# Kernel optimization log

Measured on AMD Instinct MI355X. Metric: run time of the kernel, lower is better.

## Reference

```python
import jax, jax.numpy as jnp
from jax import lax
import numpy as np

DN = ('NCHW', 'OIHW', 'NCHW')

def conv(x, w, b, stride, pad):
    y = lax.conv_general_dilated(x, w, (stride, stride), [(pad, pad), (pad, pad)], dimension_numbers=DN)
    return y if b is None else y + b[None, :, None, None]

def conv_transpose(x, w, b):
    # torch ConvTranspose2d(k=4, s=2, p=1); w in torch layout (Cin, Cout, 4, 4)
    w_f = jnp.flip(w, (2, 3)).transpose(1, 0, 2, 3)  # -> OIHW, flipped
    y = lax.conv_general_dilated(x, w_f, (1, 1), [(2, 2), (2, 2)], lhs_dilation=(2, 2), dimension_numbers=DN)
    return y + b[None, :, None, None]

def res_stack(x, w3, w1, n_layers=2):
    # shared weights across layers (ModuleList([layer]*n) aliases one module)
    for _ in range(n_layers):
        h = conv(jax.nn.relu(x), w3, None, 1, 1)
        h = conv(jax.nn.relu(h), w1, None, 1, 0)
        x = x + h
    return jax.nn.relu(x)

def setup_inputs() -> dict:
    key = jax.random.key(0)
    ks = jax.random.split(key, 16)
    s = 0.02
    d = {
        'x': jax.random.normal(ks[0], (32, 3, 256, 256), jnp.float32),
        'enc_w1': jax.random.normal(ks[1], (128, 3, 4, 4), jnp.float32) * s,
        'enc_b1': jnp.zeros((128,), jnp.float32),
        'enc_w2': jax.random.normal(ks[2], (256, 128, 4, 4), jnp.float32) * s,
        'enc_b2': jnp.zeros((256,), jnp.float32),
        'enc_w3': jax.random.normal(ks[3], (512, 256, 4, 4), jnp.float32) * s,
        'enc_b3': jnp.zeros((512,), jnp.float32),
        'enc_res_w3': jax.random.normal(ks[4], (32, 512, 3, 3), jnp.float32) * s,
        'enc_res_w1': jax.random.normal(ks[5], (512, 32, 1, 1), jnp.float32) * s,
        'prevq_w': jax.random.normal(ks[6], (64, 512, 1, 1), jnp.float32) * s,
        'prevq_b': jnp.zeros((64,), jnp.float32),
        'emb': jax.random.normal(ks[7], (512, 64), jnp.float32),
        'dec_w1': jax.random.normal(ks[8], (64, 256, 4, 4), jnp.float32) * s,
        'dec_b1': jnp.zeros((256,), jnp.float32),
        'dec_res_w3': jax.random.normal(ks[9], (32, 256, 3, 3), jnp.float32) * s,
        'dec_res_w1': jax.random.normal(ks[10], (256, 32, 1, 1), jnp.float32) * s,
        'dec_w2': jax.random.normal(ks[11], (256, 128, 4, 4), jnp.float32) * s,
        'dec_b2': jnp.zeros((128,), jnp.float32),
        'dec_w3': jax.random.normal(ks[12], (128, 3, 4, 4), jnp.float32) * s,
        'dec_b3': jnp.zeros((3,), jnp.float32),
    }
    return d

def vqvae_fwd(x, enc_w1, enc_b1, enc_w2, enc_b2, enc_w3, enc_b3, enc_res_w3, enc_res_w1,
              prevq_w, prevq_b, emb, dec_w1, dec_b1, dec_res_w3, dec_res_w1,
              dec_w2, dec_b2, dec_w3, dec_b3):
    # encoder
    z = jax.nn.relu(conv(x, enc_w1, enc_b1, 2, 1))
    z = jax.nn.relu(conv(z, enc_w2, enc_b2, 2, 1))
    z = conv(z, enc_w3, enc_b3, 2, 1)
    z = res_stack(z, enc_res_w3, enc_res_w1)
    z_e = conv(z, prevq_w, prevq_b, 1, 0)  # (B, D=64, 32, 32)
    # vector quantiser
    B, C, H, W = z_e.shape
    x_flat = z_e.reshape(B, C, H * W).transpose(0, 2, 1)  # (B, HW, D)
    d2 = (jnp.sum(x_flat ** 2, -1, keepdims=True)
          - 2.0 * jnp.einsum('bnd,kd->bnk', x_flat, emb)
          + jnp.sum(emb ** 2, -1))
    idx = jnp.argmin(d2, axis=2)  # (B, HW)
    z_q_flat = emb[idx]  # (B, HW, D)
    z_q = z_q_flat.transpose(0, 2, 1).reshape(B, C, H, W)
    sg = lax.stop_gradient
    q_loss = jnp.mean((sg(z_q_flat) - x_flat) ** 2) + jnp.mean((z_q_flat - sg(x_flat)) ** 2)
    # decoder
    y = conv_transpose(z_q, dec_w1, dec_b1)  # (B, 256, 64, 64)
    y = res_stack(y, dec_res_w3, dec_res_w1)
    y = jax.nn.relu(conv_transpose(y, dec_w2, dec_b2))
    y = conv_transpose(y, dec_w3, dec_b3)  # (B, 3, 256, 256)
    return y, q_loss

def reference(x, enc_w1, enc_b1, enc_w2, enc_b2, enc_w3, enc_b3, enc_res_w3, enc_res_w1,
              prevq_w, prevq_b, emb, dec_w1, dec_b1, dec_res_w3, dec_res_w1,
              dec_w2, dec_b2, dec_w3, dec_b3):
    return vqvae_fwd(x, enc_w1, enc_b1, enc_w2, enc_b2, enc_w3, enc_b3, enc_res_w3, enc_res_w1,
                     prevq_w, prevq_b, emb, dec_w1, dec_b1, dec_res_w3, dec_res_w1,
                     dec_w2, dec_b2, dec_w3, dec_b3)
```

## Files before the change

kernel.cpp:

```cpp
#include <hip/hip_runtime.h>
#include <hip/hip_bf16.h>

typedef __attribute__((ext_vector_type(8))) short short8;
typedef __attribute__((ext_vector_type(4))) float f32x4;
typedef __attribute__((ext_vector_type(4))) unsigned int uint4v;

__device__ __forceinline__ unsigned short f2bf(float f) {
  unsigned u = __builtin_bit_cast(unsigned, f);
  u = (u + 0x7FFFu + ((u >> 16) & 1u)) >> 16;
  return (unsigned short)u;
}
__device__ __forceinline__ float bf2f(unsigned short h) {
  unsigned u = ((unsigned)h) << 16;
  return __builtin_bit_cast(float, u);
}
__device__ __forceinline__ unsigned pk_bf16(float a, float b) {
  __hip_bfloat162 h = __float22bfloat162_rn(make_float2(a, b));
  unsigned u;
  __builtin_memcpy(&u, &h, 4);
  return u;
}

template<int TMT, int MT, int MODE, bool SPLIT, bool RELU_IN, bool RELU_OUT, bool BIAS, bool ACCUM>
__global__ __launch_bounds__(256, 4) void k_mfconv(
    const float* __restrict__ in, const unsigned short* __restrict__ wp,
    const float* __restrict__ bias, float* __restrict__ out,
    int Ci, int inW, int inH, int pWSH, int pHWSH,
    int Co, int ntap, int ntt,
    unsigned syp, unsigned sxp,
    int outW, int outHW) {
  const int tid  = threadIdx.x;
  const int lane = tid & 63, wave = tid >> 6;
  const int pW  = 1 << pWSH;
  const int pHW = 1 << pHWSH;
  const int inHW = inW * inH;
  const int nk32 = Ci >> 5;
  const int KS   = (nk32 >= 2) ? 2 : 1;
  const int NITS = 4 * KS;
  const int cpt  = nk32 / KS;
  const int total = ntap * cpt;
  constexpr int TT = TMT * MT;

  int bx = blockIdx.x;
  const int gx = gridDim.x;
  if ((gx & 7) == 0) bx = (bx & 7) * (gx >> 3) + (bx >> 3);
  const int n0  = bx * 64;
  const int coG = blockIdx.y;
  const int ph  = (MODE == 1) ? blockIdx.z : 0;
  const int tap0 = (MODE == 1) ? ph * 4 : 0;
  const int pdy = ph >> 1, pdx = ph & 1;

  constexpr int NPL = SPLIT ? 2 : 1;
  constexpr int PL = 64 * 70;
  __shared__ __align__(16) unsigned short Bs[2 * NPL * PL];

  const int px  = lane;
  const int p   = n0 + px;
  const int img = p >> pHWSH;
  const int rem = p & (pHW - 1);
  const int y   = rem >> pWSH;
  const int x   = rem & (pW - 1);
  const size_t base_img = (size_t)img * Ci * inHW;

  constexpr int NTO = (TMT == 4) ? 4 : 2;
  const int mt0 = (TMT == 4) ? wave : (wave & 1);
  const int ntb = (TMT == 4) ? 0 : ((wave >> 1) * 2);
  f32x4 acc[MT * NTO];
#pragma unroll
  for (int u = 0; u < MT * NTO; ++u) acc[u] = (f32x4){0.f, 0.f, 0.f, 0.f};

  const int cp = wave;
  float v[16];

  auto ldr = [&](int tap_, int chunk_) {
    const int T = tap0 + tap_;
    const int dy = (int)((syp >> (2 * T)) & 3u) - 1;
    const int dx = (int)((sxp >> (2 * T)) & 3u) - 1;
    const int ys = (MODE == 2) ? (2 * y + dy) : (y + dy);
    const int xs = (MODE == 2) ? (2 * x + dx) : (x + dx);
    const bool ok = ((unsigned)ys < (unsigned)inH) && ((unsigned)xs < (unsigned)inW);
    const float* __restrict__ ipb = in + base_img + (ptrdiff_t)ys * inW + xs;
    const int ci0 = chunk_ * (KS * 32);
#pragma unroll
    for (int it2 = 0; it2 < 8; ++it2) {
      if (it2 >= NITS) break;
      const int cl = 2 * (cp + 4 * it2);
      float a = 0.f, b = 0.f;
      if (ok) {
        a = ipb[(size_t)(ci0 + cl) * inHW];
        b = ipb[(size_t)(ci0 + cl + 1) * inHW];
      }
      if (RELU_IN) { a = fmaxf(a, 0.f); b = fmaxf(b, 0.f); }
      v[2 * it2] = a; v[2 * it2 + 1] = b;
    }
  };
  auto pwr = [&](int b) {
#pragma unroll
    for (int it2 = 0; it2 < 8; ++it2) {
      if (it2 >= NITS) break;
      const int cl = 2 * (cp + 4 * it2);
      float a = v[2 * it2], c = v[2 * it2 + 1];
      unsigned hp = pk_bf16(a, c);
      *(unsigned*)&Bs[(b * NPL) * PL + px * 70 + cl] = hp;
      if (SPLIT) {
        float h0 = bf2f((unsigned short)hp), h1 = bf2f((unsigned short)(hp >> 16));
        *(unsigned*)&Bs[(b * NPL + 1) * PL + px * 70 + cl] = pk_bf16(a - h0, c - h1);
      }
    }
  };

  ldr(0, 0);
  pwr(0);
  __syncthreads();

  int tap = 0, chunk = 0;
  for (int it = 0; it < total; ++it) {
    const int b = it & 1;
    const int T = tap0 + tap;
    int tap2 = tap, chunk2 = chunk + 1;
    if (chunk2 == cpt) { chunk2 = 0; tap2 = tap + 1; }
    const bool more = (it + 1 < total);
    if (more) ldr(tap2, chunk2);
#pragma unroll
    for (int s = 0; s < 2; ++s) {
      if (s >= KS) break;
      const int cic = chunk * KS + s;
      short8 ah[MT], al[MT];
#pragma unroll
      for (int m = 0; m < MT; ++m) {
        const int mtm = mt0 + m * TMT;
        size_t abase;
        if (SPLIT) abase = ((((size_t)coG * ntt + T) * nk32 + cic) * 2 * TT + mtm) * 512;
        else       abase = ((((size_t)coG * ntt + T) * nk32 + cic) * TT + mtm) * 512;
        ah[m] = *(const short8*)(wp + abase + (size_t)lane * 8);
        if (SPLIT) al[m] = *(const short8*)(wp + abase + (size_t)TT * 512 + (size_t)lane * 8);
      }
      short8 bh[NTO], bl[NTO];
#pragma unroll
      for (int u = 0; u < NTO; ++u) {
        const int row = 16 * (ntb + u) + (lane & 15);
        const unsigned* bp = (const unsigned*)&Bs[(b * NPL) * PL + row * 70 + s * 32 + (lane >> 4) * 8];
        uint4v hv = {bp[0], bp[1], bp[2], bp[3]};
        bh[u] = __builtin_bit_cast(short8, hv);
        if (SPLIT) {
          const unsigned* bpl = bp + (PL >> 1);
          uint4v lv = {bpl[0], bpl[1], bpl[2], bpl[3]};
          bl[u] = __builtin_bit_cast(short8, lv);
        }
      }
#pragma unroll
      for (int m = 0; m < MT; ++m)
#pragma unroll
        for (int u = 0; u < NTO; ++u) {
          f32x4 a = acc[m * NTO + u];
          a = __builtin_amdgcn_mfma_f32_16x16x32_bf16(ah[m], bh[u], a, 0, 0, 0);
          if (SPLIT) {
            a = __builtin_amdgcn_mfma_f32_16x16x32_bf16(al[m], bh[u], a, 0, 0, 0);
            a = __builtin_amdgcn_mfma_f32_16x16x32_bf16(ah[m], bl[u], a, 0, 0, 0);
          }
          acc[m * NTO + u] = a;
        }
    }
    if (more) {
      pwr(b ^ 1);
      __syncthreads();
    }
    tap = tap2; chunk = chunk2;
  }

#pragma unroll
  for (int m = 0; m < MT; ++m) {
    const int mtm = mt0 + m * TMT;
#pragma unroll
    for (int u = 0; u < NTO; ++u) {
      const int nt = ntb + u;
      const int pn = n0 + nt * 16 + (lane & 15);
      const int img2 = pn >> pHWSH;
      const int rem2 = pn & (pHW - 1);
      const int y2 = rem2 >> pWSH, x2 = rem2 & (pW - 1);
      int oy, ox;
      if (MODE == 1) { oy = 2 * y2 + pdy; ox = 2 * x2 + pdx; }
      else           { oy = y2;           ox = x2; }
#pragma unroll
      for (int r = 0; r < 4; ++r) {
        const int co = coG * (TT * 16) + mtm * 16 + (lane >> 4) * 4 + r;
        float val = acc[m * NTO + u][r];
        if (BIAS) val += bias[co];
        if (RELU_OUT) val = fmaxf(val, 0.f);
        size_t oi = ((size_t)img2 * Co + co) * outHW + (size_t)oy * outW + ox;
        if (ACCUM) out[oi] += val; else out[oi] = val;
      }
    }
  }
}

__global__ __launch_bounds__(256, 4) void k_mfenc1(
    const float* __restrict__ in, const unsigned short* __restrict__ wp,
    const float* __restrict__ bias, float* __restrict__ out) {
  const int tid = threadIdx.x, lane = tid & 63, wave = tid >> 6;
  int bx = blockIdx.x;
  const int gx = gridDim.x;
  if ((gx & 7) == 0) bx = (bx & 7) * (gx >> 3) + (bx >> 3);
  const int n0 = bx * 64;
  const int p = n0 + lane;
  const int img = p >> 14;
  const int rem = p & 16383;
  const int y = rem >> 7, x = rem & 127;
  __shared__ __align__(16) unsigned short Bs[2 * 4480];
  const float* __restrict__ ib = in + (size_t)img * 3 * 65536;
#pragma unroll
  for (int i = 0; i < 8; ++i) {
    const int kk0 = 2 * (wave + 4 * i);
    float vv[2];
#pragma unroll
    for (int q = 0; q < 2; ++q) {
      const int kk = kk0 + q;
      const int tap = kk >> 2, c = kk & 3;
      const int iy = 2 * y + (tap >> 2) - 1, ix = 2 * x + (tap & 3) - 1;
      const bool ok = (c < 3) && ((unsigned)iy < 256u) && ((unsigned)ix < 256u);
      vv[q] = ok ? ib[((size_t)c << 16) + (size_t)iy * 256 + ix] : 0.f;
    }
    unsigned hp = pk_bf16(vv[0], vv[1]);
    *(unsigned*)&Bs[lane * 70 + kk0] = hp;
    float h0 = bf2f((unsigned short)hp), h1 = bf2f((unsigned short)(hp >> 16));
    *(unsigned*)&Bs[4480 + lane * 70 + kk0] = pk_bf16(vv[0] - h0, vv[1] - h1);
  }
  __syncthreads();

  f32x4 acc[8];
#pragma unroll
  for (int u = 0; u < 8; ++u) acc[u] = (f32x4){0.f, 0.f, 0.f, 0.f};
#pragma unroll
  for (int s = 0; s < 2; ++s) {
    short8 ah[2], al[2];
#pragma unroll
    for (int m = 0; m < 2; ++m) {
      const int mtm = wave + m * 4;
      size_t abase = (((size_t)s * 2 + 0) * 8 + mtm) * 512;
      ah[m] = *(const short8*)(wp + abase + (size_t)lane * 8);
      al[m] = *(const short8*)(wp + abase + 8 * 512 + (size_t)lane * 8);
    }
    short8 bh[4], bl[4];
#pragma unroll
    for (int u = 0; u < 4; ++u) {
      const int row = 16 * u + (lane & 15);
      const unsigned* bp = (const unsigned*)&Bs[row * 70 + s * 32 + (lane >> 4) * 8];
      uint4v hv = {bp[0], bp[1], bp[2], bp[3]};
      bh[u] = __builtin_bit_cast(short8, hv);
      const unsigned* bpl = bp + 2240;
      uint4v lv = {bpl[0], bpl[1], bpl[2], bpl[3]};
      bl[u] = __builtin_bit_cast(short8, lv);
    }
#pragma unroll
    for (int m = 0; m < 2; ++m)
#pragma unroll
      for (int u = 0; u < 4; ++u) {
        f32x4 a = acc[m * 4 + u];
        a = __builtin_amdgcn_mfma_f32_16x16x32_bf16(ah[m], bh[u], a, 0, 0, 0);
        a = __builtin_amdgcn_mfma_f32_16x16x32_bf16(al[m], bh[u], a, 0, 0, 0);
        a = __builtin_amdgcn_mfma_f32_16x16x32_bf16(ah[m], bl[u], a, 0, 0, 0);
        acc[m * 4 + u] = a;
      }
  }
#pragma unroll
  for (int m = 0; m < 2; ++m)
#pragma unroll
    for (int u = 0; u < 4; ++u) {
      const int pn = n0 + u * 16 + (lane & 15);
      const int img2 = pn >> 14;
      const int rem2 = pn & 16383;
#pragma unroll
      for (int r = 0; r < 4; ++r) {
        const int co = (wave + m * 4) * 16 + (lane >> 4) * 4 + r;
        float val = fmaxf(acc[m * 4 + u][r] + bias[co], 0.f);
        out[((size_t)img2 * 128 + co) * 16384 + rem2] = val;
      }
    }
}

template<bool SPLIT>
__global__ __launch_bounds__(256) void k_pack_o(
    const float* __restrict__ w, unsigned short* __restrict__ p,
    int Co, int Ci, int ntap, int TMT, int E) {
  int i = blockIdx.x * 256 + threadIdx.x;
  if (i >= E) return;
  const int NC = Ci >> 5;
  int j = i & 7, lane = (i >> 3) & 63, r = i >> 9;
  int mt = r % TMT; r /= TMT;
  int sp = 0;
  if (SPLIT) { sp = r % 2; r /= 2; }
  int cic = r % NC; r /= NC;
  int T = r % ntap; int coG = r / ntap;
  int co = coG * (TMT * 16) + mt * 16 + (lane & 15);
  int ci = cic * 32 + (lane >> 4) * 8 + j;
  float wv = w[((size_t)co * Ci + ci) * ntap + T];
  unsigned short hv = f2bf(wv);
  p[i] = (SPLIT && sp == 1) ? f2bf(wv - bf2f(hv)) : hv;
}

__global__ __launch_bounds__(256) void k_pack_ct(
    const float* __restrict__ w, unsigned short* __restrict__ p,
    int Ci, int Co, int TMT, int E) {
  int i = blockIdx.x * 256 + threadIdx.x;
  if (i >= E) return;
  const int NC = Ci >> 5;
  int j = i & 7, lane = (i >> 3) & 63, r = i >> 9;
  int mt = r % TMT; r /= TMT;
  int cic = r % NC; r /= NC;
  int T = r % 16;   int coG = r / 16;
  int phx = T >> 2, t = T & 3;
  int dy = phx >> 1, dx = phx & 1, ty = t >> 1, tx = t & 1;
  int ky = 2 * ty + 1 - dy, kx = 2 * tx + 1 - dx;
  int co = coG * (TMT * 16) + mt * 16 + (lane & 15);
  int ci = cic * 32 + (lane >> 4) * 8 + j;
  p[i] = f2bf(w[(((size_t)ci * Co + co) * 4 + ky) * 4 + kx]);
}

__global__ __launch_bounds__(256) void k_pack_e1(
    const float* __restrict__ w, unsigned short* __restrict__ p) {
  int i = blockIdx.x * 256 + threadIdx.x;
  int j = i & 7, lane = (i >> 3) & 63, r = i >> 9;
  int mt = r % 8; r /= 8;
  int sp = r % 2; r /= 2;
  int cic = r;
  int co = mt * 16 + (lane & 15);
  int kk = cic * 32 + (lane >> 4) * 8 + j;
  int tap = kk >> 2, c = kk & 3;
  float wv = (c < 3) ? w[(((size_t)co * 3 + c) * 4 + (tap >> 2)) * 4 + (tap & 3)] : 0.f;
  unsigned short hv = f2bf(wv);
  p[i] = (sp == 1) ? f2bf(wv - bf2f(hv)) : hv;
}

template<int COB, bool RELU_OUT>
__global__ __launch_bounds__(256) void k_conv4(
    const float* __restrict__ in, const float* __restrict__ w,
    const float* __restrict__ bias, float* __restrict__ out,
    int N, int Ci, int Hi, int Wi, int Co) {
  const int Ho = Hi >> 1, Wo = Wi >> 1;
  const int ow = blockIdx.x * 16 + (threadIdx.x & 15);
  const int oh = blockIdx.y * 16 + (threadIdx.x >> 4);
  const int zcnt = Co / COB;
  const int co0 = (blockIdx.z % zcnt) * COB;
  const int n   = blockIdx.z / zcnt;
  if (oh >= Ho || ow >= Wo) return;
  const float* __restrict__ ip = in + (size_t)n * Ci * Hi * Wi;
  float acc[COB];
#pragma unroll
  for (int j = 0; j < COB; ++j) acc[j] = bias[co0 + j];
  const int ih0 = 2 * oh - 1, iw0 = 2 * ow - 1;
  for (int ci = 0; ci < Ci; ++ci) {
    const float* __restrict__ ic = ip + (size_t)ci * Hi * Wi;
    float v[16];
#pragma unroll
    for (int kh = 0; kh < 4; ++kh) {
      const int ih = ih0 + kh;
      const bool hok = (unsigned)ih < (unsigned)Hi;
      const float* __restrict__ irow = ic + (long)ih * Wi;
#pragma unroll
      for (int kw = 0; kw < 4; ++kw) {
        const int iw = iw0 + kw;
        v[kh * 4 + kw] = (hok && (unsigned)iw < (unsigned)Wi) ? irow[iw] : 0.f;
      }
    }
#pragma unroll
    for (int j = 0; j < COB; ++j) {
      const float* __restrict__ wc = w + ((size_t)(co0 + j) * Ci + ci) * 16;
#pragma unroll
      for (int t = 0; t < 16; ++t) acc[j] = fmaf(v[t], wc[t], acc[j]);
    }
  }
#pragma unroll
  for (int j = 0; j < COB; ++j) {
    float a = acc[j];
    if (RELU_OUT) a = fmaxf(a, 0.f);
    out[(((size_t)n * Co + co0 + j) * Ho + oh) * Wo + ow] = a;
  }
}

template<int COB, bool RELU_IN, int CSPLIT>
__global__ __launch_bounds__(256) void k_conv3(
    const float* __restrict__ in, const float* __restrict__ w,
    float* __restrict__ out, int N, int Ci, int H, int W, int Co) {
  const int ow = blockIdx.x * 16 + (threadIdx.x & 15);
  const int oh = blockIdx.y * 16 + (threadIdx.x >> 4);
  const int zcnt = Co / COB;
  const int z = blockIdx.z;
  const int cs  = z % CSPLIT;
  const int co0 = ((z / CSPLIT) % zcnt) * COB;
  const int n   = z / (CSPLIT * zcnt);
  if (oh >= H || ow >= W) return;
  const int CPS = Ci / CSPLIT;
  const float* __restrict__ ip = in + (size_t)n * Ci * H * W;
  float acc[COB];
#pragma unroll
  for (int j = 0; j < COB; ++j) acc[j] = 0.f;
  for (int ci = cs * CPS; ci < (cs + 1) * CPS; ++ci) {
    const float* __restrict__ ic = ip + (size_t)ci * H * W;
    float v[9];
#pragma unroll
    for (int kh = 0; kh < 3; ++kh) {
      const int ih = oh - 1 + kh;
      const bool hok = (unsigned)ih < (unsigned)H;
      const float* __restrict__ irow = ic + (long)ih * W;
#pragma unroll
      for (int kw = 0; kw < 3; ++kw) {
        const int iw = ow - 1 + kw;
        float t = (hok && (unsigned)iw < (unsigned)W) ? irow[iw] : 0.f;
        if (RELU_IN) t = fmaxf(t, 0.f);
        v[kh * 3 + kw] = t;
      }
    }
#pragma unroll
    for (int j = 0; j < COB; ++j) {
      const float* __restrict__ wc = w + ((size_t)(co0 + j) * Ci + ci) * 9;
#pragma unroll
      for (int t = 0; t < 9; ++t) acc[j] = fmaf(v[t], wc[t], acc[j]);
    }
  }
#pragma unroll
  for (int j = 0; j < COB; ++j) {
    size_t oi = (((size_t)n * Co + co0 + j) * H + oh) * W + ow;
    if (CSPLIT > 1) atomicAdd(&out[oi], acc[j]);
    else out[oi] = acc[j];
  }
}

template<int COB, bool RELU_IN, bool ACCUM>
__global__ __launch_bounds__(256) void k_conv1(
    const float* __restrict__ in, const float* __restrict__ w,
    const float* __restrict__ bias, float* __restrict__ out,
    int N, int Ci, int P, int Co) {
  const int p = blockIdx.x * 256 + threadIdx.x;
  const int co0 = blockIdx.y * COB;
  const int n = blockIdx.z;
  if (p >= P) return;
  float acc[COB];
#pragma unroll
  for (int j = 0; j < COB; ++j) acc[j] = bias ? bias[co0 + j] : 0.f;
  const float* __restrict__ ip = in + (size_t)n * Ci * P + p;
#pragma unroll 8
  for (int ci = 0; ci < Ci; ++ci) {
    float v = ip[(size_t)ci * P];
    if (RELU_IN) v = fmaxf(v, 0.f);
#pragma unroll
    for (int j = 0; j < COB; ++j)
      acc[j] = fmaf(v, w[(size_t)(co0 + j) * Ci + ci], acc[j]);
  }
#pragma unroll
  for (int j = 0; j < COB; ++j) {
    size_t oi = ((size_t)n * Co + co0 + j) * P + p;
    if (ACCUM) out[oi] += acc[j]; else out[oi] = acc[j];
  }
}

template<int COB, bool RELU_IN, bool RELU_OUT>
__global__ __launch_bounds__(256) void k_convT(
    const float* __restrict__ in, const float* __restrict__ w,
    const float* __restrict__ bias, float* __restrict__ out,
    int N, int Ci, int Hi, int Wi, int Co) {
  const int Ho = Hi * 2, Wo = Wi * 2;
  const int x = blockIdx.x * 16 + (threadIdx.x & 15);
  const int y = blockIdx.y * 16 + (threadIdx.x >> 4);
  const int zcnt = Co / COB;
  const int co0 = (blockIdx.z % zcnt) * COB;
  const int n   = blockIdx.z / zcnt;
  if (x >= Wi || y >= Hi) return;
  const float* __restrict__ ip = in + (size_t)n * Ci * Hi * Wi;
  float a00[COB], a01[COB], a10[COB], a11[COB];
#pragma unroll
  for (int j = 0; j < COB; ++j) {
    float b = bias[co0 + j];
    a00[j] = b; a01[j] = b; a10[j] = b; a11[j] = b;
  }
  const bool r0 = y > 0, r2 = y + 1 < Hi, c0 = x > 0, c2 = x + 1 < Wi;
#pragma unroll 2
  for (int ci = 0; ci < Ci; ++ci) {
    const float* __restrict__ ic = ip + (size_t)ci * Hi * Wi + (size_t)y * Wi + x;
    float v00 = 0.f, v01 = 0.f, v02 = 0.f, v10 = 0.f, v12 = 0.f,
          v20 = 0.f, v21 = 0.f, v22 = 0.f;
    float v11 = ic[0];
    if (c0) v10 = ic[-1];
    if (c2) v12 = ic[1];
    if (r0) { v01 = ic[-Wi]; if (c0) v00 = ic[-Wi - 1]; if (c2) v02 = ic[-Wi + 1]; }
    if (r2) { v21 = ic[Wi];  if (c0) v20 = ic[Wi - 1];  if (c2) v22 = ic[Wi + 1]; }
    if (RELU_IN) {
      v00 = fmaxf(v00, 0.f); v01 = fmaxf(v01, 0.f); v02 = fmaxf(v02, 0.f);
      v10 = fmaxf(v10, 0.f); v11 = fmaxf(v11, 0.f); v12 = fmaxf(v12, 0.f);
      v20 = fmaxf(v20, 0.f); v21 = fmaxf(v21, 0.f); v22 = fmaxf(v22, 0.f);
    }
#pragma unroll
    for (int j = 0; j < COB; ++j) {
      const float* __restrict__ wc = w + ((size_t)ci * Co + co0 + j) * 16;
      a00[j] = fmaf(v11, wc[5],  fmaf(v10, wc[7],  fmaf(v01, wc[13], fmaf(v00, wc[15], a00[j]))));
      a01[j] = fmaf(v12, wc[4],  fmaf(v11, wc[6],  fmaf(v02, wc[12], fmaf(v01, wc[14], a01[j]))));
      a10[j] = fmaf(v21, wc[1],  fmaf(v20, wc[3],  fmaf(v11, wc[9],  fmaf(v10, wc[11], a10[j]))));
      a11[j] = fmaf(v22, wc[0],  fmaf(v21, wc[2],  fmaf(v12, wc[8],  fmaf(v11, wc[10], a11[j]))));
    }
  }
#pragma unroll
  for (int j = 0; j < COB; ++j) {
    size_t b = ((size_t)n * Co + co0 + j) * Ho;
    float o00 = a00[j], o01 = a01[j], o10 = a10[j], o11 = a11[j];
    if (RELU_OUT) {
      o00 = fmaxf(o00, 0.f); o01 = fmaxf(o01, 0.f);
      o10 = fmaxf(o10, 0.f); o11 = fmaxf(o11, 0.f);
    }
    out[(b + 2 * y) * Wo + 2 * x]         = o00;
    out[(b + 2 * y) * Wo + 2 * x + 1]     = o01;
    out[(b + 2 * y + 1) * Wo + 2 * x]     = o10;
    out[(b + 2 * y + 1) * Wo + 2 * x + 1] = o11;
  }
}

__global__ __launch_bounds__(256, 2) void k_vq(
    const float* __restrict__ ze, const float* __restrict__ emb,
    float* __restrict__ zq, float* __restrict__ loss) {
  __shared__ float e2s[512];
  const int tid = threadIdx.x;
  for (int k = tid; k < 512; k += 256) {
    const f32x4* e4 = (const f32x4*)(emb + (size_t)k * 64);
    float s = 0.f;
#pragma unroll
    for (int dq = 0; dq < 16; ++dq) {
      f32x4 ev = e4[dq];
      s = fmaf(ev[0], ev[0], s); s = fmaf(ev[1], ev[1], s);
      s = fmaf(ev[2], ev[2], s); s = fmaf(ev[3], ev[3], s);
    }
    e2s[k] = s;
  }
  __syncthreads();
  const int p = blockIdx.x * 256 + tid;
  const int n = p >> 10, px = p & 1023;
  float xv[64];
  const float* __restrict__ zp = ze + (size_t)n * 64 * 1024 + px;
#pragma unroll
  for (int d = 0; d < 64; ++d) xv[d] = zp[(size_t)d * 1024];
  float best = 1e30f; int bi = 0;
  for (int k = 0; k < 512; ++k) {
    const f32x4* e4 = (const f32x4*)(emb + (size_t)k * 64);
    float dot = 0.f;
#pragma unroll
    for (int dq = 0; dq < 16; ++dq) {
      f32x4 ev = e4[dq];
      dot = fmaf(xv[4 * dq],     ev[0], dot);
      dot = fmaf(xv[4 * dq + 1], ev[1], dot);
      dot = fmaf(xv[4 * dq + 2], ev[2], dot);
      dot = fmaf(xv[4 * dq + 3], ev[3], dot);
    }
    float sc = fmaf(-2.f, dot, e2s[k]);
    if (sc < best) { best = sc; bi = k; }
  }
  const float* __restrict__ eb = emb + (size_t)bi * 64;
  float* __restrict__ qp = zq + (size_t)n * 64 * 1024 + px;
  float l = 0.f;
#pragma unroll
  for (int d = 0; d < 64; ++d) {
    float ev = eb[d];
    qp[(size_t)d * 1024] = ev;
    float df = ev - xv[d];
    l = fmaf(df, df, l);
  }
#pragma unroll
  for (int off = 32; off > 0; off >>= 1) l += __shfl_down(l, off, 64);
  if ((tid & 63) == 0) atomicAdd(loss, l * (2.f / 2097152.f));
}

__global__ __launch_bounds__(64) void k_vq64(
    const float* __restrict__ ze, const float* __restrict__ emb,
    float* __restrict__ zq, float* __restrict__ loss,
    int N, int P, int K) {
  const int t = blockIdx.x * 64 + threadIdx.x;
  if (t >= N * P) return;
  const int n = t / P, p = t % P;
  float xv[64];
  const float* __restrict__ zp = ze + (size_t)n * 64 * P + p;
#pragma unroll
  for (int d = 0; d < 64; ++d) xv[d] = zp[(size_t)d * P];
  float best = 1e30f; int bi = 0;
  for (int k = 0; k < K; ++k) {
    const float* __restrict__ e = emb + (size_t)k * 64;
    float dot = 0.f, e2 = 0.f;
#pragma unroll
    for (int d = 0; d < 64; ++d) {
      float ev = e[d];
      dot = fmaf(xv[d], ev, dot);
      e2  = fmaf(ev, ev, e2);
    }
    float score = e2 - 2.f * dot;
    if (score < best) { best = score; bi = k; }
  }
  const float* __restrict__ eb = emb + (size_t)bi * 64;
  float* __restrict__ qp = zq + (size_t)n * 64 * P + p;
  float l = 0.f;
#pragma unroll
  for (int d = 0; d < 64; ++d) {
    float ev = eb[d];
    qp[(size_t)d * P] = ev;
    float df = ev - xv[d];
    l = fmaf(df, df, l);
  }
#pragma unroll
  for (int off = 32; off > 0; off >>= 1) l += __shfl_down(l, off, 64);
  if ((threadIdx.x & 63) == 0) atomicAdd(loss, l * (2.f / 2097152.f));
}

extern "C" void kernel_launch(void* const* d_in, const int* in_sizes, int n_in,
                              void* d_out, int out_size, void* d_ws, size_t ws_size,
                              hipStream_t stream) {
  const float* x    = (const float*)d_in[0];
  const float* ew1  = (const float*)d_in[1];
  const float* eb1  = (const float*)d_in[2];
  const float* ew2  = (const float*)d_in[3];
  const float* eb2  = (const float*)d_in[4];
  const float* ew3  = (const float*)d_in[5];
  const float* eb3  = (const float*)d_in[6];
  const float* erw3 = (const float*)d_in[7];
  const float* erw1 = (const float*)d_in[8];
  const float* pqw  = (const float*)d_in[9];
  const float* pqb  = (const float*)d_in[10];
  const float* emb  = (const float*)d_in[11];
  const float* dw1  = (const float*)d_in[12];
  const float* db1  = (const float*)d_in[13];
  const float* drw3 = (const float*)d_in[14];
  const float* drw1 = (const float*)d_in[15];
  const float* dw2  = (const float*)d_in[16];
  const float* db2  = (const float*)d_in[17];
  const float* dw3  = (const float*)d_in[18];
  const float* db3  = (const float*)d_in[19];
  float* out = (float*)d_out;
  char*  ws  = (char*)d_ws;
  float* loss = out + 6291456;
  const size_t MiB = 1048576ull, KiB = 1024ull;

  dim3 blk(256);
  hipMemsetAsync(loss, 0, 4, stream);

  unsigned syct = 0, sxct = 0;
  for (int T = 0; T < 16; ++T) {
    int phx = T >> 2, dy = phx >> 1, dx = phx & 1, t = T & 3, ty = t >> 1, tx = t & 1;
    int sy = (dy == 0) ? (ty ? -1 : 0) : (ty ? 0 : 1);
    int sx = (dx == 0) ? (tx ? -1 : 0) : (tx ? 0 : 1);
    syct |= (unsigned)(sy + 1) << (2 * T);
    sxct |= (unsigned)(sx + 1) << (2 * T);
  }
  unsigned syc3 = 0, sxc3 = 0;
  for (int t = 0; t < 9; ++t) {
    syc3 |= (unsigned)(t / 3) << (2 * t);
    sxc3 |= (unsigned)(t % 3) << (2 * t);
  }
  unsigned syc4 = 0, sxc4 = 0;
  for (int t = 0; t < 16; ++t) {
    syc4 |= (unsigned)(t / 4) << (2 * t);
    sxc4 |= (unsigned)(t % 4) << (2 * t);
  }
  const unsigned sy1 = 1, sx1 = 1;

  auto packs = [&](char* PB) {
    unsigned short* e2p   = (unsigned short*)(PB);
    unsigned short* e3p   = (unsigned short*)(PB + 2048 * KiB);
    unsigned short* erc3p = (unsigned short*)(PB + 10240 * KiB);
    unsigned short* erc1p = (unsigned short*)(PB + 10816 * KiB);
    unsigned short* pqp   = (unsigned short*)(PB + 10880 * KiB);
    unsigned short* d1p   = (unsigned short*)(PB + 11008 * KiB);
    unsigned short* d2p   = (unsigned short*)(PB + 11520 * KiB);
    unsigned short* dc3p  = (unsigned short*)(PB + 12544 * KiB);
    unsigned short* dc1p  = (unsigned short*)(PB + 12688 * KiB);
    unsigned short* e1p   = (unsigned short*)(PB + 12704 * KiB);
    k_pack_o<true ><<<dim3(1048576 / 256), blk, 0, stream>>>(ew2,  e2p,  256, 128, 16, 8, 1048576);
    k_pack_o<true ><<<dim3(4194304 / 256), blk, 0, stream>>>(ew3,  e3p,  512, 256, 16, 8, 4194304);
    k_pack_o<true ><<<dim3(294912 / 256),  blk, 0, stream>>>(erw3, erc3p, 32, 512,  9, 2, 294912);
    k_pack_o<true ><<<dim3(32768 / 256),   blk, 0, stream>>>(erw1, erc1p, 512, 32,  1, 8, 32768);
    k_pack_o<true ><<<dim3(65536 / 256),   blk, 0, stream>>>(pqw,  pqp,   64, 512,  1, 4, 65536);
    k_pack_ct<<<dim3(262144 / 256), blk, 0, stream>>>(dw1, d1p, 64, 256, 8, 262144);
    k_pack_ct<<<dim3(524288 / 256), blk, 0, stream>>>(dw2, d2p, 256, 128, 8, 524288);
    k_pack_o<false><<<dim3(73728 / 256),   blk, 0, stream>>>(drw3, dc3p,  32, 256,  9, 2, 73728);
    k_pack_o<false><<<dim3(8192 / 256),    blk, 0, stream>>>(drw1, dc1p, 256, 32,  1, 8, 8192);
    k_pack_e1<<<dim3(256), blk, 0, stream>>>(ew1, e1p);
  };

  if (ws_size >= 498ull * MiB) {
    float* z1 = (float*)ws;
    float* z2 = (float*)(ws + 256 * MiB);
    float* z3 = (float*)(ws + 384 * MiB);
    float* h  = (float*)(ws + 448 * MiB);
    float* ze = (float*)(ws + 452 * MiB);
    float* zq = (float*)(ws + 460 * MiB);
    float* hd = (float*)(ws + 468 * MiB);
    char*  PB = ws + 484 * MiB;
    unsigned short* e2p   = (unsigned short*)(PB);
    unsigned short* e3p   = (unsigned short*)(PB + 2048 * KiB);
    unsigned short* erc3p = (unsigned short*)(PB + 10240 * KiB);
    unsigned short* erc1p = (unsigned short*)(PB + 10816 * KiB);
    unsigned short* pqp   = (unsigned short*)(PB + 10880 * KiB);
    unsigned short* d1p   = (unsigned short*)(PB + 11008 * KiB);
    unsigned short* d2p   = (unsigned short*)(PB + 11520 * KiB);
    unsigned short* dc3p  = (unsigned short*)(PB + 12544 * KiB);
    unsigned short* dc1p  = (unsigned short*)(PB + 12688 * KiB);
    unsigned short* e1p   = (unsigned short*)(PB + 12704 * KiB);
    packs(PB);

    k_mfenc1<<<dim3(8192), blk, 0, stream>>>(x, e1p, eb1, z1);
    k_mfconv<4, 2, 2, true, false, true, true, false><<<dim3(2048, 2), blk, 0, stream>>>(
        z1, e2p, eb2, z2, 128, 128, 128, 6, 12, 256, 16, 16, syc4, sxc4, 64, 4096);
    k_mfconv<4, 2, 2, true, false, false, true, false><<<dim3(512, 4), blk, 0, stream>>>(
        z2, e3p, eb3, z3, 256, 64, 64, 5, 10, 512, 16, 16, syc4, sxc4, 32, 1024);
    for (int i = 0; i < 2; ++i) {
      k_mfconv<2, 1, 0, true, true, false, false, false><<<dim3(512, 1), blk, 0, stream>>>(
          z3, erc3p, nullptr, h, 512, 32, 32, 5, 10, 32, 9, 9, syc3, sxc3, 32, 1024);
      k_mfconv<4, 2, 0, true, true, false, false, true><<<dim3(512, 4), blk, 0, stream>>>(
          h, erc1p, nullptr, z3, 32, 32, 32, 5, 10, 512, 1, 1, sy1, sx1, 32, 1024);
    }
    k_mfconv<4, 1, 0, true, true, false, true, false><<<dim3(512, 1), blk, 0, stream>>>(
        z3, pqp, pqb, ze, 512, 32, 32, 5, 10, 64, 1, 1, sy1, sx1, 32, 1024);
    k_vq<<<dim3(128), blk, 0, stream>>>(ze, emb, zq, loss);
    float* y1 = (float*)(ws + 256 * MiB);
    float* y2 = (float*)ws;
    k_mfconv<4, 2, 1, false, false, false, true, false><<<dim3(512, 2, 4), blk, 0, stream>>>(
        zq, d1p, db1, y1, 64, 32, 32, 5, 10, 256, 4, 16, syct, sxct, 64, 4096);
    for (int i = 0; i < 2; ++i) {
      k_mfconv<2, 1, 0, false, true, false, false, false><<<dim3(2048, 1), blk, 0, stream>>>(
          y1, dc3p, nullptr, hd, 256, 64, 64, 6, 12, 32, 9, 9, syc3, sxc3, 64, 4096);
      k_mfconv<4, 2, 0, false, true, false, false, true><<<dim3(2048, 2), blk, 0, stream>>>(
          hd, dc1p, nullptr, y1, 32, 64, 64, 6, 12, 256, 1, 1, sy1, sx1, 64, 4096);
    }
    k_mfconv<4, 2, 1, false, true, true, true, false><<<dim3(2048, 1, 4), blk, 0, stream>>>(
        y1, d2p, db2, y2, 256, 64, 64, 6, 12, 128, 4, 16, syct, sxct, 128, 16384);
    k_convT<3, false, false><<<dim3(8, 8, 32), blk, 0, stream>>>(y2, dw3, db3, out, 32, 128, 128, 128, 3);
    return;
  }

  if (ws_size >= 128ull * MiB) {
    float* z3  = (float*)ws;
    float* h   = (float*)(ws + 64 * MiB);
    float* ze  = (float*)(ws + 68 * MiB);
    float* zq  = (float*)(ws + 100 * MiB);
    char*  PB  = ws + 115 * MiB;
    unsigned short* e2p   = (unsigned short*)(PB);
    unsigned short* e3p   = (unsigned short*)(PB + 2048 * KiB);
    unsigned short* erc3p = (unsigned short*)(PB + 10240 * KiB);
    unsigned short* erc1p = (unsigned short*)(PB + 10816 * KiB);
    unsigned short* pqp   = (unsigned short*)(PB + 10880 * KiB);
    unsigned short* d1p   = (unsigned short*)(PB + 11008 * KiB);
    unsigned short* d2p   = (unsigned short*)(PB + 11520 * KiB);
    unsigned short* dc3p  = (unsigned short*)(PB + 12544 * KiB);
    unsigned short* dc1p  = (unsigned short*)(PB + 12688 * KiB);
    unsigned short* e1p   = (unsigned short*)(PB + 12704 * KiB);
    packs(PB);

    const int NE = 4;
    float* z1c = (float*)(ws + 64 * MiB);
    float* z2c = (float*)(ws + 96 * MiB);
    for (int n0 = 0; n0 < 32; n0 += NE) {
      const float* xb = x + (size_t)n0 * 3 * 65536;
      float* z3b = z3 + (size_t)n0 * 512 * 1024;
      k_mfenc1<<<dim3(NE * 256), blk, 0, stream>>>(xb, e1p, eb1, z1c);
      k_mfconv<4, 2, 2, true, false, true, true, false><<<dim3(256, 2), blk, 0, stream>>>(
          z1c, e2p, eb2, z2c, 128, 128, 128, 6, 12, 256, 16, 16, syc4, sxc4, 64, 4096);
      k_mfconv<4, 2, 2, true, false, false, true, false><<<dim3(64, 4), blk, 0, stream>>>(
          z2c, e3p, eb3, z3b, 256, 64, 64, 5, 10, 512, 16, 16, syc4, sxc4, 32, 1024);
    }
    for (int i = 0; i < 2; ++i) {
      k_mfconv<2, 1, 0, true, true, false, false, false><<<dim3(512, 1), blk, 0, stream>>>(
          z3, erc3p, nullptr, h, 512, 32, 32, 5, 10, 32, 9, 9, syc3, sxc3, 32, 1024);
      k_mfconv<4, 2, 0, true, true, false, false, true><<<dim3(512, 4), blk, 0, stream>>>(
          h, erc1p, nullptr, z3, 32, 32, 32, 5, 10, 512, 1, 1, sy1, sx1, 32, 1024);
    }
    k_mfconv<4, 1, 0, true, true, false, true, false><<<dim3(512, 1), blk, 0, stream>>>(
        z3, pqp, pqb, ze, 512, 32, 32, 5, 10, 64, 1, 1, sy1, sx1, 32, 1024);
    k_vq<<<dim3(128), blk, 0, stream>>>(ze, emb, zq, loss);

    const int ND = 8;
    float* y1c = (float*)ws;
    float* hd  = (float*)(ws + 32 * MiB);
    float* y2c = (float*)(ws + 36 * MiB);
    for (int c = 0; c < 32; c += ND) {
      const float* zqb = zq + (size_t)c * 64 * 1024;
      float* outb = out + (size_t)c * 3 * 65536;
      k_mfconv<4, 2, 1, false, false, false, true, false><<<dim3(128, 2, 4), blk, 0, stream>>>(
          zqb, d1p, db1, y1c, 64, 32, 32, 5, 10, 256, 4, 16, syct, sxct, 64, 4096);
      for (int i = 0; i < 2; ++i) {
        k_mfconv<2, 1, 0, false, true, false, false, false><<<dim3(512, 1), blk, 0, stream>>>(
            y1c, dc3p, nullptr, hd, 256, 64, 64, 6, 12, 32, 9, 9, syc3, sxc3, 64, 4096);
        k_mfconv<4, 2, 0, false, true, false, false, true><<<dim3(512, 2), blk, 0, stream>>>(
            hd, dc1p, nullptr, y1c, 32, 64, 64, 6, 12, 256, 1, 1, sy1, sx1, 64, 4096);
      }
      k_mfconv<4, 2, 1, false, true, true, true, false><<<dim3(512, 1, 4), blk, 0, stream>>>(
          y1c, d2p, db2, y2c, 256, 64, 64, 6, 12, 128, 4, 16, syct, sxct, 128, 16384);
      k_convT<3, false, false><<<dim3(8, 8, ND), blk, 0, stream>>>(y2c, dw3, db3, outb, ND, 128, 128, 128, 3);
    }
    return;
  }

  const size_t PER_IMG = 12582912ull;
  int NB = (int)(ws_size / PER_IMG);
  if (NB > 32) NB = 32;
  if (NB < 1)  NB = 1;

  for (int n0 = 0; n0 < 32; n0 += NB) {
    const int nb = (32 - n0 < NB) ? (32 - n0) : NB;
    const float* xb   = x   + (size_t)n0 * 3 * 65536;
    float*       outb = out + (size_t)n0 * 3 * 65536;

    float* z1 = (float*)ws;
    float* z2 = (float*)(ws + (size_t)NB * 8388608ull);
    float* z3 = (float*)ws;
    char*  tb = ws + (size_t)NB * 2097152ull;
    float* he = (float*)tb;
    float* ze = (float*)(tb + (size_t)NB * 131072ull);
    float* zq = (float*)(tb + (size_t)NB * 393216ull);
    float* hd = (float*)(tb + (size_t)NB * 655360ull);
    float* y1 = z2;
    float* y2 = (float*)ws;

    k_conv4<4, true ><<<dim3(8, 8, nb * 32), blk, 0, stream>>>(xb, ew1, eb1, z1, nb,   3, 256, 256, 128);
    k_conv4<4, true ><<<dim3(4, 4, nb * 64), blk, 0, stream>>>(z1, ew2, eb2, z2, nb, 128, 128, 128, 256);
    k_conv4<4, false><<<dim3(2, 2, nb * 128), blk, 0, stream>>>(z2, ew3, eb3, z3, nb, 256,  64,  64, 512);
    for (int i = 0; i < 2; ++i) {
      k_conv3<4, true, 1><<<dim3(2, 2, nb * 8), blk, 0, stream>>>(z3, erw3, he, nb, 512, 32, 32, 32);
      k_conv1<8, true, true><<<dim3(4, 64, nb), blk, 0, stream>>>(he, erw1, nullptr, z3, nb, 32, 1024, 512);
    }
    k_conv1<8, true, false><<<dim3(4, 8, nb), blk, 0, stream>>>(z3, pqw, pqb, ze, nb, 512, 1024, 64);
    k_vq64<<<dim3(nb * 16), dim3(64), 0, stream>>>(ze, emb, zq, loss, nb, 1024, 512);
    k_convT<4, false, false><<<dim3(2, 2, nb * 64), blk, 0, stream>>>(zq, dw1, db1, y1, nb,  64, 32, 32, 256);
    for (int i = 0; i < 2; ++i) {
      k_conv3<4, true, 1><<<dim3(4, 4, nb * 8), blk, 0, stream>>>(y1, drw3, hd, nb, 256, 64, 64, 32);
      k_conv1<8, true, true><<<dim3(16, 32, nb), blk, 0, stream>>>(hd, drw1, nullptr, y1, nb, 32, 4096, 256);
    }
    k_convT<4, true, true ><<<dim3(4, 4, nb * 32), blk, 0, stream>>>(y1, dw2, db2, y2, nb, 256, 64, 64, 128);
    k_convT<1, false, false><<<dim3(8, 8, nb * 3), blk, 0, stream>>>(y2, dw3, db3, outb, nb, 128, 128, 128, 3);
  }
}
```

Measured before the change: 4.290 ms.

## Split-K low-occupancy convs with atomics; run final ConvTranspose on MFMA path

```diff
diff --git a/kernel.cpp b/kernel.cpp
--- a/kernel.cpp
+++ b/kernel.cpp
@@ -21,14 +21,14 @@
   return u;
 }
 
-template<int TMT, int MT, int MODE, bool SPLIT, bool RELU_IN, bool RELU_OUT, bool BIAS, bool ACCUM>
+template<int TMT, int MT, int MODE, int ZSP, bool SPLIT, bool RELU_IN, bool RELU_OUT, bool BIAS, int SM>
 __global__ __launch_bounds__(256, 4) void k_mfconv(
     const float* __restrict__ in, const unsigned short* __restrict__ wp,
     const float* __restrict__ bias, float* __restrict__ out,
     int Ci, int inW, int inH, int pWSH, int pHWSH,
     int Co, int ntap, int ntt,
     unsigned syp, unsigned sxp,
-    int outW, int outHW) {
+    int outW, int outHW, int CoSt) {
   const int tid  = threadIdx.x;
   const int lane = tid & 63, wave = tid >> 6;
   const int pW  = 1 << pWSH;
@@ -50,6 +50,13 @@
   const int tap0 = (MODE == 1) ? ph * 4 : 0;
   const int pdy = ph >> 1, pdx = ph & 1;
 
+  int it0 = 0, itEnd = total;
+  if (MODE != 1 && ZSP > 1) {
+    const int per = total / ZSP;
+    it0 = blockIdx.z * per;
+    itEnd = it0 + per;
+  }
+
   constexpr int NPL = SPLIT ? 2 : 1;
   constexpr int PL = 64 * 70;
   __shared__ __align__(16) unsigned short Bs[2 * NPL * PL];
@@ -109,17 +116,17 @@
     }
   };
 
-  ldr(0, 0);
+  int tap = it0 / cpt, chunk = it0 % cpt;
+  ldr(tap, chunk);
   pwr(0);
   __syncthreads();
 
-  int tap = 0, chunk = 0;
-  for (int it = 0; it < total; ++it) {
-    const int b = it & 1;
+  for (int it = it0; it < itEnd; ++it) {
+    const int b = (it - it0) & 1;
     const int T = tap0 + tap;
     int tap2 = tap, chunk2 = chunk + 1;
     if (chunk2 == cpt) { chunk2 = 0; tap2 = tap + 1; }
-    const bool more = (it + 1 < total);
+    const bool more = (it + 1 < itEnd);
     if (more) ldr(tap2, chunk2);
 #pragma unroll
     for (int s = 0; s < 2; ++s) {
@@ -184,11 +191,15 @@
 #pragma unroll
       for (int r = 0; r < 4; ++r) {
         const int co = coG * (TT * 16) + mtm * 16 + (lane >> 4) * 4 + r;
-        float val = acc[m * NTO + u][r];
-        if (BIAS) val += bias[co];
-        if (RELU_OUT) val = fmaxf(val, 0.f);
-        size_t oi = ((size_t)img2 * Co + co) * outHW + (size_t)oy * outW + ox;
-        if (ACCUM) out[oi] += val; else out[oi] = val;
+        if (co < CoSt) {
+          float val = acc[m * NTO + u][r];
+          if (BIAS) val += bias[co];
+          if (RELU_OUT) val = fmaxf(val, 0.f);
+          size_t oi = ((size_t)img2 * Co + co) * outHW + (size_t)oy * outW + ox;
+          if (SM == 0) out[oi] = val;
+          else if (SM == 1) out[oi] += val;
+          else atomicAdd(&out[oi], val);
+        }
       }
     }
   }
@@ -300,7 +311,7 @@
 
 __global__ __launch_bounds__(256) void k_pack_ct(
     const float* __restrict__ w, unsigned short* __restrict__ p,
-    int Ci, int Co, int TMT, int E) {
+    int Ci, int CoR, int TMT, int E) {
   int i = blockIdx.x * 256 + threadIdx.x;
   if (i >= E) return;
   const int NC = Ci >> 5;
@@ -313,7 +324,8 @@
   int ky = 2 * ty + 1 - dy, kx = 2 * tx + 1 - dx;
   int co = coG * (TMT * 16) + mt * 16 + (lane & 15);
   int ci = cic * 32 + (lane >> 4) * 8 + j;
-  p[i] = f2bf(w[(((size_t)ci * Co + co) * 4 + ky) * 4 + kx]);
+  float wv = (co < CoR) ? w[(((size_t)ci * CoR + co) * 4 + ky) * 4 + kx] : 0.f;
+  p[i] = f2bf(wv);
 }
 
 __global__ __launch_bounds__(256) void k_pack_e1(
@@ -514,6 +526,7 @@
 
 __global__ __launch_bounds__(256, 2) void k_vq(
     const float* __restrict__ ze, const float* __restrict__ emb,
+    const float* __restrict__ qb,
     float* __restrict__ zq, float* __restrict__ loss) {
   __shared__ float e2s[512];
   const int tid = threadIdx.x;
@@ -534,7 +547,7 @@
   float xv[64];
   const float* __restrict__ zp = ze + (size_t)n * 64 * 1024 + px;
 #pragma unroll
-  for (int d = 0; d < 64; ++d) xv[d] = zp[(size_t)d * 1024];
+  for (int d = 0; d < 64; ++d) xv[d] = zp[(size_t)d * 1024] + (qb ? qb[d] : 0.f);
   float best = 1e30f; int bi = 0;
   for (int k = 0; k < 512; ++k) {
     const f32x4* e4 = (const f32x4*)(emb + (size_t)k * 64);
@@ -666,6 +679,7 @@
     unsigned short* dc3p  = (unsigned short*)(PB + 12544 * KiB);
     unsigned short* dc1p  = (unsigned short*)(PB + 12688 * KiB);
     unsigned short* e1p   = (unsigned short*)(PB + 12704 * KiB);
+    unsigned short* d3p   = (unsigned short*)(PB + 12832 * KiB);
     k_pack_o<true ><<<dim3(1048576 / 256), blk, 0, stream>>>(ew2,  e2p,  256, 128, 16, 8, 1048576);
     k_pack_o<true ><<<dim3(4194304 / 256), blk, 0, stream>>>(ew3,  e3p,  512, 256, 16, 8, 4194304);
     k_pack_o<true ><<<dim3(294912 / 256),  blk, 0, stream>>>(erw3, erc3p, 32, 512,  9, 2, 294912);
@@ -676,6 +690,7 @@
     k_pack_o<false><<<dim3(73728 / 256),   blk, 0, stream>>>(drw3, dc3p,  32, 256,  9, 2, 73728);
     k_pack_o<false><<<dim3(8192 / 256),    blk, 0, stream>>>(drw1, dc1p, 256, 32,  1, 8, 8192);
     k_pack_e1<<<dim3(256), blk, 0, stream>>>(ew1, e1p);
+    k_pack_ct<<<dim3(65536 / 256), blk, 0, stream>>>(dw3, d3p, 128, 3, 2, 65536);
   };
 
   if (ws_size >= 498ull * MiB) {
@@ -697,35 +712,40 @@
     unsigned short* dc3p  = (unsigned short*)(PB + 12544 * KiB);
     unsigned short* dc1p  = (unsigned short*)(PB + 12688 * KiB);
     unsigned short* e1p   = (unsigned short*)(PB + 12704 * KiB);
+    unsigned short* d3p   = (unsigned short*)(PB + 12832 * KiB);
     packs(PB);
 
     k_mfenc1<<<dim3(8192), blk, 0, stream>>>(x, e1p, eb1, z1);
-    k_mfconv<4, 2, 2, true, false, true, true, false><<<dim3(2048, 2), blk, 0, stream>>>(
-        z1, e2p, eb2, z2, 128, 128, 128, 6, 12, 256, 16, 16, syc4, sxc4, 64, 4096);
-    k_mfconv<4, 2, 2, true, false, false, true, false><<<dim3(512, 4), blk, 0, stream>>>(
-        z2, e3p, eb3, z3, 256, 64, 64, 5, 10, 512, 16, 16, syc4, sxc4, 32, 1024);
+    k_mfconv<4, 2, 2, 1, true, false, true, true, 0><<<dim3(2048, 2), blk, 0, stream>>>(
+        z1, e2p, eb2, z2, 128, 128, 128, 6, 12, 256, 16, 16, syc4, sxc4, 64, 4096, 256);
+    k_mfconv<4, 2, 2, 1, true, false, false, true, 0><<<dim3(512, 4), blk, 0, stream>>>(
+        z2, e3p, eb3, z3, 256, 64, 64, 5, 10, 512, 16, 16, syc4, sxc4, 32, 1024, 512);
     for (int i = 0; i < 2; ++i) {
-      k_mfconv<2, 1, 0, true, true, false, false, false><<<dim3(512, 1), blk, 0, stream>>>(
-          z3, erc3p, nullptr, h, 512, 32, 32, 5, 10, 32, 9, 9, syc3, sxc3, 32, 1024);
-      k_mfconv<4, 2, 0, true, true, false, false, true><<<dim3(512, 4), blk, 0, stream>>>(
-          h, erc1p, nullptr, z3, 32, 32, 32, 5, 10, 512, 1, 1, sy1, sx1, 32, 1024);
-    }
-    k_mfconv<4, 1, 0, true, true, false, true, false><<<dim3(512, 1), blk, 0, stream>>>(
-        z3, pqp, pqb, ze, 512, 32, 32, 5, 10, 64, 1, 1, sy1, sx1, 32, 1024);
-    k_vq<<<dim3(128), blk, 0, stream>>>(ze, emb, zq, loss);
+      hipMemsetAsync(h, 0, 4 * MiB, stream);
+      k_mfconv<2, 1, 0, 3, true, true, false, false, 2><<<dim3(512, 1, 3), blk, 0, stream>>>(
+          z3, erc3p, nullptr, h, 512, 32, 32, 5, 10, 32, 9, 9, syc3, sxc3, 32, 1024, 32);
+      k_mfconv<4, 2, 0, 1, true, true, false, false, 1><<<dim3(512, 4), blk, 0, stream>>>(
+          h, erc1p, nullptr, z3, 32, 32, 32, 5, 10, 512, 1, 1, sy1, sx1, 32, 1024, 512);
+    }
+    hipMemsetAsync(ze, 0, 8 * MiB, stream);
+    k_mfconv<4, 1, 0, 4, true, true, false, false, 2><<<dim3(512, 1, 4), blk, 0, stream>>>(
+        z3, pqp, nullptr, ze, 512, 32, 32, 5, 10, 64, 1, 1, sy1, sx1, 32, 1024, 64);
+    k_vq<<<dim3(128), blk, 0, stream>>>(ze, emb, pqb, zq, loss);
     float* y1 = (float*)(ws + 256 * MiB);
     float* y2 = (float*)ws;
-    k_mfconv<4, 2, 1, false, false, false, true, false><<<dim3(512, 2, 4), blk, 0, stream>>>(
-        zq, d1p, db1, y1, 64, 32, 32, 5, 10, 256, 4, 16, syct, sxct, 64, 4096);
+    k_mfconv<4, 2, 1, 1, false, false, false, true, 0><<<dim3(512, 2, 4), blk, 0, stream>>>(
+        zq, d1p, db1, y1, 64, 32, 32, 5, 10, 256, 4, 16, syct, sxct, 64, 4096, 256);
     for (int i = 0; i < 2; ++i) {
-      k_mfconv<2, 1, 0, false, true, false, false, false><<<dim3(2048, 1), blk, 0, stream>>>(
-          y1, dc3p, nullptr, hd, 256, 64, 64, 6, 12, 32, 9, 9, syc3, sxc3, 64, 4096);
-      k_mfconv<4, 2, 0, false, true, false, false, true><<<dim3(2048, 2), blk, 0, stream>>>(
-          hd, dc1p, nullptr, y1, 32, 64, 64, 6, 12, 256, 1, 1, sy1, sx1, 64, 4096);
-    }
-    k_mfconv<4, 2, 1, false, true, true, true, false><<<dim3(2048, 1, 4), blk, 0, stream>>>(
-        y1, d2p, db2, y2, 256, 64, 64, 6, 12, 128, 4, 16, syct, sxct, 128, 16384);
-    k_convT<3, false, false><<<dim3(8, 8, 32), blk, 0, stream>>>(y2, dw3, db3, out, 32, 128, 128, 128, 3);
+      hipMemsetAsync(hd, 0, 16 * MiB, stream);
+      k_mfconv<2, 1, 0, 3, false, true, false, false, 2><<<dim3(2048, 1, 3), blk, 0, stream>>>(
+          y1, dc3p, nullptr, hd, 256, 64, 64, 6, 12, 32, 9, 9, syc3, sxc3, 64, 4096, 32);
+      k_mfconv<4, 2, 0, 1, false, true, false, false, 1><<<dim3(2048, 2), blk, 0, stream>>>(
+          hd, dc1p, nullptr, y1, 32, 64, 64, 6, 12, 256, 1, 1, sy1, sx1, 64, 4096, 256);
+    }
+    k_mfconv<4, 2, 1, 1, false, true, true, true, 0><<<dim3(2048, 1, 4), blk, 0, stream>>>(
+        y1, d2p, db2, y2, 256, 64, 64, 6, 12, 128, 4, 16, syct, sxct, 128, 16384, 128);
+    k_mfconv<2, 1, 1, 1, false, false, false, true, 0><<<dim3(8192, 1, 4), blk, 0, stream>>>(
+        y2, d3p, db3, out, 128, 128, 128, 7, 14, 3, 4, 16, syct, sxct, 256, 65536, 3);
     return;
   }
 
@@ -745,6 +765,7 @@
     unsigned short* dc3p  = (unsigned short*)(PB + 12544 * KiB);
     unsigned short* dc1p  = (unsigned short*)(PB + 12688 * KiB);
     unsigned short* e1p   = (unsigned short*)(PB + 12704 * KiB);
+    unsigned short* d3p   = (unsigned short*)(PB + 12832 * KiB);
     packs(PB);
 
     const int NE = 4;
@@ -754,20 +775,22 @@
       const float* xb = x + (size_t)n0 * 3 * 65536;
       float* z3b = z3 + (size_t)n0 * 512 * 1024;
       k_mfenc1<<<dim3(NE * 256), blk, 0, stream>>>(xb, e1p, eb1, z1c);
-      k_mfconv<4, 2, 2, true, false, true, true, false><<<dim3(256, 2), blk, 0, stream>>>(
-          z1c, e2p, eb2, z2c, 128, 128, 128, 6, 12, 256, 16, 16, syc4, sxc4, 64, 4096);
-      k_mfconv<4, 2, 2, true, false, false, true, false><<<dim3(64, 4), blk, 0, stream>>>(
-          z2c, e3p, eb3, z3b, 256, 64, 64, 5, 10, 512, 16, 16, syc4, sxc4, 32, 1024);
+      k_mfconv<4, 2, 2, 1, true, false, true, true, 0><<<dim3(256, 2), blk, 0, stream>>>(
+          z1c, e2p, eb2, z2c, 128, 128, 128, 6, 12, 256, 16, 16, syc4, sxc4, 64, 4096, 256);
+      k_mfconv<4, 2, 2, 1, true, false, false, true, 0><<<dim3(64, 4), blk, 0, stream>>>(
+          z2c, e3p, eb3, z3b, 256, 64, 64, 5, 10, 512, 16, 16, syc4, sxc4, 32, 1024, 512);
     }
     for (int i = 0; i < 2; ++i) {
-      k_mfconv<2, 1, 0, true, true, false, false, false><<<dim3(512, 1), blk, 0, stream>>>(
-          z3, erc3p, nullptr, h, 512, 32, 32, 5, 10, 32, 9, 9, syc3, sxc3, 32, 1024);
-      k_mfconv<4, 2, 0, true, true, false, false, true><<<dim3(512, 4), blk, 0, stream>>>(
-          h, erc1p, nullptr, z3, 32, 32, 32, 5, 10, 512, 1, 1, sy1, sx1, 32, 1024);
-    }
-    k_mfconv<4, 1, 0, true, true, false, true, false><<<dim3(512, 1), blk, 0, stream>>>(
-        z3, pqp, pqb, ze, 512, 32, 32, 5, 10, 64, 1, 1, sy1, sx1, 32, 1024);
-    k_vq<<<dim3(128), blk, 0, stream>>>(ze, emb, zq, loss);
+      hipMemsetAsync(h, 0, 4 * MiB, stream);
+      k_mfconv<2, 1, 0, 3, true, true, false, false, 2><<<dim3(512, 1, 3), blk, 0, stream>>>(
+          z3, erc3p, nullptr, h, 512, 32, 32, 5, 10, 32, 9, 9, syc3, sxc3, 32, 1024, 32);
+      k_mfconv<4, 2, 0, 1, true, true, false, false, 1><<<dim3(512, 4), blk, 0, stream>>>(
+          h, erc1p, nullptr, z3, 32, 32, 32, 5, 10, 512, 1, 1, sy1, sx1, 32, 1024, 512);
+    }
+    hipMemsetAsync(ze, 0, 8 * MiB, stream);
+    k_mfconv<4, 1, 0, 4, true, true, false, false, 2><<<dim3(512, 1, 4), blk, 0, stream>>>(
+        z3, pqp, nullptr, ze, 512, 32, 32, 5, 10, 64, 1, 1, sy1, sx1, 32, 1024, 64);
+    k_vq<<<dim3(128), blk, 0, stream>>>(ze, emb, pqb, zq, loss);
 
     const int ND = 8;
     float* y1c = (float*)ws;
@@ -776,17 +799,19 @@
     for (int c = 0; c < 32; c += ND) {
       const float* zqb = zq + (size_t)c * 64 * 1024;
       float* outb = out + (size_t)c * 3 * 65536;
-      k_mfconv<4, 2, 1, false, false, false, true, false><<<dim3(128, 2, 4), blk, 0, stream>>>(
-          zqb, d1p, db1, y1c, 64, 32, 32, 5, 10, 256, 4, 16, syct, sxct, 64, 4096);
+      k_mfconv<4, 2, 1, 1, false, false, false, true, 0><<<dim3(128, 2, 4), blk, 0, stream>>>(
+          zqb, d1p, db1, y1c, 64, 32, 32, 5, 10, 256, 4, 16, syct, sxct, 64, 4096, 256);
       for (int i = 0; i < 2; ++i) {
-        k_mfconv<2, 1, 0, false, true, false, false, false><<<dim3(512, 1), blk, 0, stream>>>(
-            y1c, dc3p, nullptr, hd, 256, 64, 64, 6, 12, 32, 9, 9, syc3, sxc3, 64, 4096);
-        k_mfconv<4, 2, 0, false, true, false, false, true><<<dim3(512, 2), blk, 0, stream>>>(
-            hd, dc1p, nullptr, y1c, 32, 64, 64, 6, 12, 256, 1, 1, sy1, sx1, 64, 4096);
-      }
-      k_mfconv<4, 2, 1, false, true, true, true, false><<<dim3(512, 1, 4), blk, 0, stream>>>(
-          y1c, d2p, db2, y2c, 256, 64, 64, 6, 12, 128, 4, 16, syct, sxct, 128, 16384);
-      k_convT<3, false, false><<<dim3(8, 8, ND), blk, 0, stream>>>(y2c, dw3, db3, outb, ND, 128, 128, 128, 3);
+        hipMemsetAsync(hd, 0, 4 * MiB, stream);
+        k_mfconv<2, 1, 0, 3, false, true, false, false, 2><<<dim3(512, 1, 3), blk, 0, stream>>>(
+            y1c, dc3p, nullptr, hd, 256, 64, 64, 6, 12, 32, 9, 9, syc3, sxc3, 64, 4096, 32);
+        k_mfconv<4, 2, 0, 1, false, true, false, false, 1><<<dim3(512, 2), blk, 0, stream>>>(
+            hd, dc1p, nullptr, y1c, 32, 64, 64, 6, 12, 256, 1, 1, sy1, sx1, 64, 4096, 256);
+      }
+      k_mfconv<4, 2, 1, 1, false, true, true, true, 0><<<dim3(512, 1, 4), blk, 0, stream>>>(
+          y1c, d2p, db2, y2c, 256, 64, 64, 6, 12, 128, 4, 16, syct, sxct, 128, 16384, 128);
+      k_mfconv<2, 1, 1, 1, false, false, false, true, 0><<<dim3(2048, 1, 4), blk, 0, stream>>>(
+          y2c, d3p, db3, outb, 128, 128, 128, 7, 14, 3, 4, 16, syct, sxct, 256, 65536, 3);
     }
     return;
   }
```

New measurement: 4.172 ms. 1.03x faster.
